# Kernel optimization log

Measured on AMD Instinct MI355X. Metric: run time of the kernel, lower is better.

## Reference

```python
import jax, jax.numpy as jnp
import numpy as np

B = 64; PAST = 128; FUTURE = 64; HID = 64; HEADS = 4
F = 16 + 8 + 24 + 3  # out_preprocess = 51


def _pre(cat, num, emb0, emb1, emb2):
    # pre_processing: embedding lookups per categorical column + last 3 float cols
    return jnp.concatenate([emb0[cat[:, 0]], emb1[cat[:, 1]], emb2[cat[:, 2]], num], axis=-1)


def _gat_conv(x, edge_index, lin_w, att_src, att_dst, bias, heads, out_ch):
    # PyG GATConv: concat=False (head mean), add_self_loops=True, leaky_relu slope 0.2
    N = x.shape[0]
    loops = jnp.arange(N, dtype=edge_index.dtype)
    src = jnp.concatenate([edge_index[0], loops])
    dst = jnp.concatenate([edge_index[1], loops])
    h = (x @ lin_w).reshape(N, heads, out_ch)          # [N, H, C]
    a_src = (h * att_src).sum(-1)                      # [N, H]
    a_dst = (h * att_dst).sum(-1)
    e = jax.nn.leaky_relu(a_src[src] + a_dst[dst], 0.2)  # [E, H]
    m = jax.lax.stop_gradient(jax.ops.segment_max(e, dst, num_segments=N))
    ex = jnp.exp(e - m[dst])
    s = jax.ops.segment_sum(ex, dst, num_segments=N)
    alpha = ex / (s[dst] + 1e-16)                      # softmax over in-edges per node
    out = jax.ops.segment_sum(alpha[:, :, None] * h[src], dst, num_segments=N)
    return out.mean(1) + bias                          # concat=False -> mean over heads


def setup_inputs() -> dict:
    ks = jax.random.split(jax.random.key(0), 17)
    N1, N2 = B * PAST, B * FUTURE
    E1, E2 = N1 * 16, N2 * 16
    return dict(
        cat1=jax.random.randint(ks[0], (N1, 3), 0, 7),
        num1=jax.random.normal(ks[1], (N1, 3), dtype=jnp.float32),
        cat2=jax.random.randint(ks[2], (N2, 3), 0, 7),
        num2=jax.random.normal(ks[3], (N2, 3), dtype=jnp.float32),
        e1=jax.random.randint(ks[4], (2, E1), 0, N1),
        e2=jax.random.randint(ks[5], (2, E2), 0, N2),
        A=jax.random.randint(ks[6], (PAST + FUTURE, PAST + FUTURE), 0, 2),
        emb0=0.1 * jax.random.normal(ks[7], (24, 16), dtype=jnp.float32),
        emb1=0.1 * jax.random.normal(ks[8], (7, 8), dtype=jnp.float32),
        emb2=0.1 * jax.random.normal(ks[9], (500, 24), dtype=jnp.float32),
        g1_lin=0.1 * jax.random.normal(ks[10], (F, HEADS * (F - 1)), dtype=jnp.float32),
        g1_asrc=0.1 * jax.random.normal(ks[11], (HEADS, F - 1), dtype=jnp.float32),
        g1_adst=0.1 * jax.random.normal(ks[12], (HEADS, F - 1), dtype=jnp.float32),
        g1_b=jnp.zeros((F - 1,), dtype=jnp.float32),
        g2_lin=0.1 * jax.random.normal(ks[13], (F, HEADS), dtype=jnp.float32),
        g2_asrc=0.1 * jax.random.normal(ks[14], (HEADS, 1), dtype=jnp.float32),
        g2_adst=0.1 * jax.random.normal(ks[15], (HEADS, 1), dtype=jnp.float32),
        g2_b=jnp.zeros((1,), dtype=jnp.float32),
        W=0.1 * jax.random.normal(ks[16], (F - 1, HID), dtype=jnp.float32),
    )


def reference(cat1, num1, cat2, num2, e1, e2, A, emb0, emb1, emb2,
              g1_lin, g1_asrc, g1_adst, g1_b, g2_lin, g2_asrc, g2_adst, g2_b, W):
    x = _pre(cat1, num1, emb0, emb1, emb2)                       # [B*PAST, F]
    x2 = _pre(cat2, num2, emb0, emb1, emb2).reshape(B, FUTURE, F)
    x1 = _gat_conv(x, e1, g1_lin, g1_asrc, g1_adst, g1_b, HEADS, F - 1).reshape(B, PAST, F - 1)
    # pairwise diff between every (future, past) node pair within a graph
    diff = x1[:, None, :, :] - x2[:, :, None, :F - 1]            # [B, FUTURE, PAST, F-1]
    M = W @ W.T
    M = M + M.T                                                  # WW^T + (WW^T)^T
    # original builds full [PAST, PAST] quadratic form and extracts diagonal;
    # compute only the diagonal: -0.5 * diff_i M diff_i
    alpha = -0.5 * jnp.einsum('bfpd,de,bfpe->bfp', diff, M, diff)
    mask = A[:PAST, PAST:].T                                     # [FUTURE, PAST]
    alpha = jnp.where(mask == 0, -jnp.inf, alpha)
    alpha = jax.nn.softmax(alpha, axis=-1)
    y_past = x.reshape(B, PAST, F)[:, :, -1:]                    # [B, PAST, 1]
    tmp = alpha @ y_past                                         # [B, FUTURE, 1]
    x2b = jnp.concatenate([x2[:, :, :F - 1], tmp], axis=-1)
    out = _gat_conv(x2b.reshape(-1, F), e2, g2_lin, g2_asrc, g2_adst, g2_b, HEADS, 1)
    return out.reshape(B, FUTURE)
```

## Files before the change

### kernel.cpp

```cpp
#include <hip/hip_runtime.h>

static constexpr int B_ = 64, PAST = 128, FUTURE = 64, F_ = 51;
static constexpr int N1 = B_ * PAST;
static constexpr int N2 = B_ * FUTURE;
static constexpr int E1 = N1 * 16;
static constexpr int E2 = N2 * 16;
static constexpr int MAXDEG = 64;
static constexpr int CSR_TOT = E1 + N1 + E2 + N2 + FUTURE * PAST;

__device__ __forceinline__
float node_feat(const int* cat, const float* num, const float* e0, const float* e1,
                const float* e2, int n, int t) {
    if (t < 16) return e0[cat[n * 3 + 0] * 16 + t];
    if (t < 24) return e1[cat[n * 3 + 1] * 8 + (t - 16)];
    if (t < 48) return e2[cat[n * 3 + 2] * 24 + (t - 24)];
    return num[n * 3 + (t - 48)];
}

__global__ __launch_bounds__(256) void k_prep(
        const int* __restrict__ cat1, const float* __restrict__ num1,
        const int* __restrict__ cat2, const float* __restrict__ num2,
        const float* __restrict__ emb0, const float* __restrict__ emb1,
        const float* __restrict__ emb2,
        const float* __restrict__ g1_lin, const float* __restrict__ g1_asrc,
        const float* __restrict__ g1_adst, const float* __restrict__ W,
        float* __restrict__ h1, float* __restrict__ asrc1, float* __restrict__ adst1,
        float* __restrict__ y1, float* __restrict__ x2g, float* __restrict__ P2,
        int* __restrict__ countall) {
    __shared__ float xrow[F_];
    __shared__ float redS[200];
    __shared__ float redD[200];
    int blk = blockIdx.x, t = threadIdx.x;
    if (blk >= N1) {
        int n = blk - N1;
        if (n < 48) countall[n * 256 + t] = 0;
        if (t < F_) {
            float xv = node_feat(cat2, num2, emb0, emb1, emb2, n, t);
            xrow[t] = xv;
            x2g[n * F_ + t] = xv;
        }
        __syncthreads();
        if (t < 64) {
            float acc = 0.f;
            for (int j = 0; j < 50; ++j) acc += xrow[j] * W[j * 64 + t];
            P2[n * 64 + t] = acc;
        }
        return;
    }
    int n = blk;
    if (t < F_) {
        float xv = node_feat(cat1, num1, emb0, emb1, emb2, n, t);
        xrow[t] = xv;
        if (t == 50) y1[n] = xv;
    }
    __syncthreads();
    if (t < 200) {
        float acc = 0.f;
        for (int j = 0; j < F_; ++j) acc += xrow[j] * g1_lin[j * 200 + t];
        h1[n * 200 + t] = acc;
        redS[t] = acc * g1_asrc[t];
        redD[t] = acc * g1_adst[t];
    }
    __syncthreads();
    if (t < 4) {
        float s = 0.f;
        for (int c = 0; c < 50; ++c) s += redS[t * 50 + c];
        asrc1[n * 4 + t] = s;
    } else if (t < 8) {
        int h = t - 4;
        float s = 0.f;
        for (int c = 0; c < 50; ++c) s += redD[h * 50 + c];
        adst1[n * 4 + h] = s;
    }
}

__global__ __launch_bounds__(256) void k_csr(
        const int* __restrict__ e1, const int* __restrict__ e2,
        const int* __restrict__ A,
        int* __restrict__ count1, int* __restrict__ slot1,
        int* __restrict__ count2, int* __restrict__ slot2,
        int* __restrict__ maskT) {
    int i = blockIdx.x * blockDim.x + threadIdx.x;
    if (i < E1) {
        int src = e1[i], dst = e1[E1 + i];
        int pos = atomicAdd(&count1[dst], 1);
        if (pos < MAXDEG) slot1[dst * MAXDEG + pos] = src;
    } else if (i < E1 + N1) {
        int n = i - E1;
        int pos = atomicAdd(&count1[n], 1);
        if (pos < MAXDEG) slot1[n * MAXDEG + pos] = n;
    } else if (i < E1 + N1 + E2) {
        int k = i - E1 - N1;
        int src = e2[k], dst = e2[E2 + k];
        int pos = atomicAdd(&count2[dst], 1);
        if (pos < MAXDEG) slot2[dst * MAXDEG + pos] = src;
    } else if (i < E1 + N1 + E2 + N2) {
        int n = i - E1 - N1 - E2;
        int pos = atomicAdd(&count2[n], 1);
        if (pos < MAXDEG) slot2[n * MAXDEG + pos] = n;
    } else if (i < CSR_TOT) {
        int k = i - (E1 + N1 + E2 + N2);
        int f = k >> 7, pp = k & 127;
        maskT[k] = A[pp * 192 + PAST + f];
    }
}

__global__ __launch_bounds__(256) void k_gat1(
        const int* __restrict__ count1, const int* __restrict__ slot1,
        const float* __restrict__ h1, const float* __restrict__ asrc1,
        const float* __restrict__ adst1, const float* __restrict__ g1_b,
        const float* __restrict__ W, float* __restrict__ P1) {
    __shared__ int   Ssrc[4][64];
    __shared__ float Sw[4][4][64];
    __shared__ float Sx[4][64];
    int t = threadIdx.x, lane = t & 63, wv = t >> 6;
    int n = (blockIdx.x * 256 + t) >> 6;
    int deg = min(count1[n], MAXDEG);
    int my_src = (lane < deg) ? slot1[n * MAXDEG + lane] : 0;
    float ad0 = adst1[n * 4 + 0], ad1 = adst1[n * 4 + 1];
    float ad2 = adst1[n * 4 + 2], ad3 = adst1[n * 4 + 3];
    float ex0 = 0.f, ex1 = 0.f, ex2 = 0.f, ex3 = 0.f;
    if (lane < deg) {
        float e0 = asrc1[my_src * 4 + 0] + ad0;
        float e1 = asrc1[my_src * 4 + 1] + ad1;
        float e2 = asrc1[my_src * 4 + 2] + ad2;
        float e3 = asrc1[my_src * 4 + 3] + ad3;
        e0 = e0 >= 0.f ? e0 : 0.2f * e0;  ex0 = __expf(e0);
        e1 = e1 >= 0.f ? e1 : 0.2f * e1;  ex1 = __expf(e1);
        e2 = e2 >= 0.f ? e2 : 0.2f * e2;  ex2 = __expf(e2);
        e3 = e3 >= 0.f ? e3 : 0.2f * e3;  ex3 = __expf(e3);
    }
    float s0 = ex0, s1 = ex1, s2 = ex2, s3 = ex3;
    #pragma unroll
    for (int m = 32; m >= 1; m >>= 1) {
        s0 += __shfl_xor(s0, m);
        s1 += __shfl_xor(s1, m);
        s2 += __shfl_xor(s2, m);
        s3 += __shfl_xor(s3, m);
    }
    Ssrc[wv][lane] = my_src;
    Sw[wv][0][lane] = ex0 / (s0 + 1e-16f);
    Sw[wv][1][lane] = ex1 / (s1 + 1e-16f);
    Sw[wv][2][lane] = ex2 / (s2 + 1e-16f);
    Sw[wv][3][lane] = ex3 / (s3 + 1e-16f);
    __syncthreads();
    float acc0 = 0.f, acc1 = 0.f, acc2 = 0.f, acc3 = 0.f;
    for (int i = 0; i < deg; ++i) {
        int srci = Ssrc[wv][i];
        float w0 = Sw[wv][0][i], w1 = Sw[wv][1][i];
        float w2 = Sw[wv][2][i], w3 = Sw[wv][3][i];
        if (lane < 50) {
            const float* hr = &h1[srci * 200];
            acc0 += w0 * hr[lane];
            acc1 += w1 * hr[50 + lane];
            acc2 += w2 * hr[100 + lane];
            acc3 += w3 * hr[150 + lane];
        }
    }
    if (lane < 50)
        Sx[wv][lane] = 0.25f * (acc0 + acc1 + acc2 + acc3) + g1_b[lane];
    __syncthreads();
    float a = 0.f;
    for (int j = 0; j < 50; ++j) a += Sx[wv][j] * W[j * 64 + lane];
    P1[n * 64 + lane] = a;
}

__global__ __launch_bounds__(256) void k_attn(
        const float* __restrict__ P1, const float* __restrict__ P2,
        const int* __restrict__ maskT, const float* __restrict__ y1,
        const float* __restrict__ x2g, const float* __restrict__ g2_lin,
        float* __restrict__ h2g) {
    __shared__ float P1s[64 * 129];
    __shared__ float ys[128];
    int b = blockIdx.x >> 2, fg = blockIdx.x & 3;
    int t = threadIdx.x, lane = t & 63, wv = t >> 6;
    const float* P1b = P1 + b * 8192;
    for (int i = t; i < 8192; i += 256) {
        int pp = i >> 6, kk = i & 63;
        P1s[kk * 129 + pp] = P1b[i];
    }
    if (t < 128) ys[t] = y1[b * 128 + t];
    __syncthreads();
    for (int j = 0; j < 4; ++j) {
        int f = fg * 16 + wv * 4 + j;
        int q = b * 64 + f;
        float p2k = P2[q * 64 + lane];
        float d2a = 0.f, d2b = 0.f;
        for (int k = 0; k < 64; ++k) {
            float bk = __shfl(p2k, k);
            float va = P1s[k * 129 + lane] - bk;
            float vb = P1s[k * 129 + 64 + lane] - bk;
            d2a += va * va;
            d2b += vb * vb;
        }
        int ma = maskT[f * 128 + lane];
        int mb = maskT[f * 128 + 64 + lane];
        float va = ma ? -d2a : -1e30f;
        float vb = mb ? -d2b : -1e30f;
        float mx = fmaxf(va, vb);
        #pragma unroll
        for (int m = 32; m >= 1; m >>= 1) mx = fmaxf(mx, __shfl_xor(mx, m));
        float wa = ma ? __expf(va - mx) : 0.f;
        float wb = mb ? __expf(vb - mx) : 0.f;
        float sw = wa + wb;
        float sy = wa * ys[lane] + wb * ys[64 + lane];
        #pragma unroll
        for (int m = 32; m >= 1; m >>= 1) {
            sw += __shfl_xor(sw, m);
            sy += __shfl_xor(sy, m);
        }
        float tsh = sy / sw;
        float xv = (lane < 50) ? x2g[q * F_ + lane] : 0.f;
        #pragma unroll
        for (int h = 0; h < 4; ++h) {
            float c = xv * g2_lin[lane * 4 + h];
            #pragma unroll
            for (int m = 32; m >= 1; m >>= 1) c += __shfl_xor(c, m);
            c += tsh * g2_lin[50 * 4 + h];
            if (lane == h) h2g[q * 4 + h] = c;
        }
    }
}

__global__ __launch_bounds__(256) void k_gat2(
        const int* __restrict__ count2, const int* __restrict__ slot2,
        const float* __restrict__ h2g, const float* __restrict__ g2_asrc,
        const float* __restrict__ g2_adst, const float* __restrict__ g2_b,
        float* __restrict__ out) {
    int wave = (blockIdx.x * blockDim.x + threadIdx.x) >> 6;
    int lane = threadIdx.x & 63;
    if (wave >= N2) return;
    int n = wave;
    int deg = min(count2[n], MAXDEG);
    int my_src = (lane < deg) ? slot2[n * MAXDEG + lane] : 0;
    float ex[4], nm[4], adterm[4], as[4];
    #pragma unroll
    for (int h = 0; h < 4; ++h) {
        as[h] = g2_asrc[h];
        adterm[h] = h2g[n * 4 + h] * g2_adst[h];
        ex[h] = 0.f; nm[h] = 0.f;
    }
    if (lane < deg) {
        #pragma unroll
        for (int h = 0; h < 4; ++h) {
            float hs = h2g[my_src * 4 + h];
            float e = hs * as[h] + adterm[h];
            e = e >= 0.f ? e : 0.2f * e;
            float xv = __expf(e);
            ex[h] = xv;
            nm[h] = xv * hs;
        }
    }
    #pragma unroll
    for (int m = 32; m >= 1; m >>= 1) {
        #pragma unroll
        for (int h = 0; h < 4; ++h) {
            ex[h] += __shfl_xor(ex[h], m);
            nm[h] += __shfl_xor(nm[h], m);
        }
    }
    if (lane == 0) {
        float o = 0.f;
        #pragma unroll
        for (int h = 0; h < 4; ++h) o += nm[h] / (ex[h] + 1e-16f);
        out[n] = 0.25f * o + g2_b[0];
    }
}

extern "C" void kernel_launch(void* const* d_in, const int* in_sizes, int n_in,
                              void* d_out, int out_size, void* d_ws, size_t ws_size,
                              hipStream_t stream) {
    const int*   cat1    = (const int*)  d_in[0];
    const float* num1    = (const float*)d_in[1];
    const int*   cat2    = (const int*)  d_in[2];
    const float* num2    = (const float*)d_in[3];
    const int*   e1      = (const int*)  d_in[4];
    const int*   e2      = (const int*)  d_in[5];
    const int*   A       = (const int*)  d_in[6];
    const float* emb0    = (const float*)d_in[7];
    const float* emb1    = (const float*)d_in[8];
    const float* emb2    = (const float*)d_in[9];
    const float* g1_lin  = (const float*)d_in[10];
    const float* g1_asrc = (const float*)d_in[11];
    const float* g1_adst = (const float*)d_in[12];
    const float* g1_b    = (const float*)d_in[13];
    const float* g2_lin  = (const float*)d_in[14];
    const float* g2_asrc = (const float*)d_in[15];
    const float* g2_adst = (const float*)d_in[16];
    const float* g2_b    = (const float*)d_in[17];
    const float* W       = (const float*)d_in[18];
    float* out = (float*)d_out;

    int*   count1 = (int*)d_ws;
    int*   count2 = count1 + N1;
    int*   slot1  = count2 + N2;
    int*   slot2  = slot1 + N1 * MAXDEG;
    int*   maskT  = slot2 + N2 * MAXDEG;
    float* h1     = (float*)(maskT + FUTURE * PAST);
    float* asrc1  = h1 + N1 * 200;
    float* adst1  = asrc1 + N1 * 4;
    float* y1     = adst1 + N1 * 4;
    float* x2g    = y1 + N1;
    float* P1     = x2g + N2 * F_;
    float* P2     = P1 + N1 * 64;
    float* h2g    = P2 + N2 * 64;

    k_prep<<<N1 + N2, 256, 0, stream>>>(cat1, num1, cat2, num2, emb0, emb1, emb2,
                                        g1_lin, g1_asrc, g1_adst, W,
                                        h1, asrc1, adst1, y1, x2g, P2, count1);
    k_csr<<<CSR_TOT / 256, 256, 0, stream>>>(e1, e2, A, count1, slot1, count2, slot2, maskT);
    k_gat1<<<N1 / 4, 256, 0, stream>>>(count1, slot1, h1, asrc1, adst1, g1_b, W, P1);
    k_attn<<<B_ * 4, 256, 0, stream>>>(P1, P2, maskT, y1, x2g, g2_lin, h2g);
    k_gat2<<<N2 / 4, 256, 0, stream>>>(count2, slot2, h2g, g2_asrc, g2_adst, g2_b, out);
}
```

Measured before the change: 160.3 us.

## Fuse CSR build into prep kernel and expand distance via dot products

Merges the CSR/mask build into the prep kernel as extra blocks, with the degree counters zeroed by a memset beforehand. The future-side linear term for the second GAT is moved into prep. k_gat1 now writes P1 transposed plus per-node squared norms, so k_attn computes 2·dot − |p1|² instead of explicit squared differences (the |p2|² term cancels in the softmax). k_attn loads P1 with float4, uses one future row per wave, and launches 4x more blocks. This saves one launch, removes the transpose in shared memory, and raises parallelism. The cost is strided global writes in gat1 and the numerical differences that come from the norm expansion.

```diff
diff --git a/kernel.cpp b/kernel.cpp
--- a/kernel.cpp
+++ b/kernel.cpp
@@ -7,6 +7,7 @@
 static constexpr int E2 = N2 * 16;
 static constexpr int MAXDEG = 64;
 static constexpr int CSR_TOT = E1 + N1 + E2 + N2 + FUTURE * PAST;
+static constexpr int NB_CSR = CSR_TOT / 256;
 
 __device__ __forceinline__
 float node_feat(const int* cat, const float* num, const float* e0, const float* e1,
@@ -24,16 +25,47 @@
         const float* __restrict__ emb2,
         const float* __restrict__ g1_lin, const float* __restrict__ g1_asrc,
         const float* __restrict__ g1_adst, const float* __restrict__ W,
+        const float* __restrict__ g2_lin,
+        const int* __restrict__ e1, const int* __restrict__ e2,
+        const int* __restrict__ A,
         float* __restrict__ h1, float* __restrict__ asrc1, float* __restrict__ adst1,
         float* __restrict__ y1, float* __restrict__ x2g, float* __restrict__ P2,
-        int* __restrict__ countall) {
+        float* __restrict__ h2b,
+        int* __restrict__ count1, int* __restrict__ slot1,
+        int* __restrict__ count2, int* __restrict__ slot2, int* __restrict__ maskT) {
+    int blk = blockIdx.x, t = threadIdx.x;
+    if (blk < NB_CSR) {
+        int i = blk * 256 + t;
+        if (i < E1) {
+            int src = e1[i], dst = e1[E1 + i];
+            int pos = atomicAdd(&count1[dst], 1);
+            if (pos < MAXDEG) slot1[dst * MAXDEG + pos] = src;
+        } else if (i < E1 + N1) {
+            int n = i - E1;
+            int pos = atomicAdd(&count1[n], 1);
+            if (pos < MAXDEG) slot1[n * MAXDEG + pos] = n;
+        } else if (i < E1 + N1 + E2) {
+            int k = i - E1 - N1;
+            int src = e2[k], dst = e2[E2 + k];
+            int pos = atomicAdd(&count2[dst], 1);
+            if (pos < MAXDEG) slot2[dst * MAXDEG + pos] = src;
+        } else if (i < E1 + N1 + E2 + N2) {
+            int n = i - E1 - N1 - E2;
+            int pos = atomicAdd(&count2[n], 1);
+            if (pos < MAXDEG) slot2[n * MAXDEG + pos] = n;
+        } else if (i < CSR_TOT) {
+            int k = i - (E1 + N1 + E2 + N2);
+            int f = k >> 7, pp = k & 127;
+            maskT[k] = A[pp * 192 + PAST + f];
+        }
+        return;
+    }
     __shared__ float xrow[F_];
     __shared__ float redS[200];
     __shared__ float redD[200];
-    int blk = blockIdx.x, t = threadIdx.x;
-    if (blk >= N1) {
-        int n = blk - N1;
-        if (n < 48) countall[n * 256 + t] = 0;
+    int rb = blk - NB_CSR;
+    if (rb >= N1) {
+        int n = rb - N1;
         if (t < F_) {
             float xv = node_feat(cat2, num2, emb0, emb1, emb2, n, t);
             xrow[t] = xv;
@@ -44,10 +76,15 @@
             float acc = 0.f;
             for (int j = 0; j < 50; ++j) acc += xrow[j] * W[j * 64 + t];
             P2[n * 64 + t] = acc;
+        } else if (t < 68) {
+            int h = t - 64;
+            float acc = 0.f;
+            for (int j = 0; j < 50; ++j) acc += xrow[j] * g2_lin[j * 4 + h];
+            h2b[n * 4 + h] = acc;
         }
         return;
     }
-    int n = blk;
+    int n = rb;
     if (t < F_) {
         float xv = node_feat(cat1, num1, emb0, emb1, emb2, n, t);
         xrow[t] = xv;
@@ -74,45 +111,15 @@
     }
 }
 
-__global__ __launch_bounds__(256) void k_csr(
-        const int* __restrict__ e1, const int* __restrict__ e2,
-        const int* __restrict__ A,
-        int* __restrict__ count1, int* __restrict__ slot1,
-        int* __restrict__ count2, int* __restrict__ slot2,
-        int* __restrict__ maskT) {
-    int i = blockIdx.x * blockDim.x + threadIdx.x;
-    if (i < E1) {
-        int src = e1[i], dst = e1[E1 + i];
-        int pos = atomicAdd(&count1[dst], 1);
-        if (pos < MAXDEG) slot1[dst * MAXDEG + pos] = src;
-    } else if (i < E1 + N1) {
-        int n = i - E1;
-        int pos = atomicAdd(&count1[n], 1);
-        if (pos < MAXDEG) slot1[n * MAXDEG + pos] = n;
-    } else if (i < E1 + N1 + E2) {
-        int k = i - E1 - N1;
-        int src = e2[k], dst = e2[E2 + k];
-        int pos = atomicAdd(&count2[dst], 1);
-        if (pos < MAXDEG) slot2[dst * MAXDEG + pos] = src;
-    } else if (i < E1 + N1 + E2 + N2) {
-        int n = i - E1 - N1 - E2;
-        int pos = atomicAdd(&count2[n], 1);
-        if (pos < MAXDEG) slot2[n * MAXDEG + pos] = n;
-    } else if (i < CSR_TOT) {
-        int k = i - (E1 + N1 + E2 + N2);
-        int f = k >> 7, pp = k & 127;
-        maskT[k] = A[pp * 192 + PAST + f];
-    }
-}
-
 __global__ __launch_bounds__(256) void k_gat1(
         const int* __restrict__ count1, const int* __restrict__ slot1,
         const float* __restrict__ h1, const float* __restrict__ asrc1,
         const float* __restrict__ adst1, const float* __restrict__ g1_b,
-        const float* __restrict__ W, float* __restrict__ P1) {
-    __shared__ int   Ssrc[4][64];
-    __shared__ float Sw[4][4][64];
-    __shared__ float Sx[4][64];
+        const float* __restrict__ W, float* __restrict__ P1T,
+        float* __restrict__ n1w) {
+    __shared__ int    Ssrc[4][64];
+    __shared__ float4 Sw[4][64];
+    __shared__ float  Sx[4][64];
     int t = threadIdx.x, lane = t & 63, wv = t >> 6;
     int n = (blockIdx.x * 256 + t) >> 6;
     int deg = min(count1[n], MAXDEG);
@@ -139,22 +146,19 @@
         s3 += __shfl_xor(s3, m);
     }
     Ssrc[wv][lane] = my_src;
-    Sw[wv][0][lane] = ex0 / (s0 + 1e-16f);
-    Sw[wv][1][lane] = ex1 / (s1 + 1e-16f);
-    Sw[wv][2][lane] = ex2 / (s2 + 1e-16f);
-    Sw[wv][3][lane] = ex3 / (s3 + 1e-16f);
+    Sw[wv][lane] = make_float4(ex0 / (s0 + 1e-16f), ex1 / (s1 + 1e-16f),
+                               ex2 / (s2 + 1e-16f), ex3 / (s3 + 1e-16f));
     __syncthreads();
     float acc0 = 0.f, acc1 = 0.f, acc2 = 0.f, acc3 = 0.f;
     for (int i = 0; i < deg; ++i) {
         int srci = Ssrc[wv][i];
-        float w0 = Sw[wv][0][i], w1 = Sw[wv][1][i];
-        float w2 = Sw[wv][2][i], w3 = Sw[wv][3][i];
+        float4 w = Sw[wv][i];
         if (lane < 50) {
             const float* hr = &h1[srci * 200];
-            acc0 += w0 * hr[lane];
-            acc1 += w1 * hr[50 + lane];
-            acc2 += w2 * hr[100 + lane];
-            acc3 += w3 * hr[150 + lane];
+            acc0 += w.x * hr[lane];
+            acc1 += w.y * hr[50 + lane];
+            acc2 += w.z * hr[100 + lane];
+            acc3 += w.w * hr[150 + lane];
         }
     }
     if (lane < 50)
@@ -162,64 +166,65 @@
     __syncthreads();
     float a = 0.f;
     for (int j = 0; j < 50; ++j) a += Sx[wv][j] * W[j * 64 + lane];
-    P1[n * 64 + lane] = a;
+    int b = n >> 7, p = n & 127;
+    P1T[b * 8192 + lane * 128 + p] = a;
+    float sq = a * a;
+    #pragma unroll
+    for (int m = 32; m >= 1; m >>= 1) sq += __shfl_xor(sq, m);
+    if (lane == 0) n1w[n] = sq;
 }
 
 __global__ __launch_bounds__(256) void k_attn(
-        const float* __restrict__ P1, const float* __restrict__ P2,
+        const float* __restrict__ P1T, const float* __restrict__ P2,
         const int* __restrict__ maskT, const float* __restrict__ y1,
-        const float* __restrict__ x2g, const float* __restrict__ g2_lin,
-        float* __restrict__ h2g) {
-    __shared__ float P1s[64 * 129];
-    __shared__ float ys[128];
-    int b = blockIdx.x >> 2, fg = blockIdx.x & 3;
+        const float* __restrict__ n1w, const float* __restrict__ h2b,
+        const float* __restrict__ g2_lin, float* __restrict__ h2g) {
+    __shared__ __align__(16) float P1s[8192];
+    __shared__ __align__(16) float ys[128];
+    __shared__ __align__(16) float n1s[128];
+    int b = blockIdx.x >> 4, fg = blockIdx.x & 15;
     int t = threadIdx.x, lane = t & 63, wv = t >> 6;
-    const float* P1b = P1 + b * 8192;
-    for (int i = t; i < 8192; i += 256) {
-        int pp = i >> 6, kk = i & 63;
-        P1s[kk * 129 + pp] = P1b[i];
-    }
-    if (t < 128) ys[t] = y1[b * 128 + t];
-    __syncthreads();
-    for (int j = 0; j < 4; ++j) {
-        int f = fg * 16 + wv * 4 + j;
-        int q = b * 64 + f;
-        float p2k = P2[q * 64 + lane];
-        float d2a = 0.f, d2b = 0.f;
-        for (int k = 0; k < 64; ++k) {
-            float bk = __shfl(p2k, k);
-            float va = P1s[k * 129 + lane] - bk;
-            float vb = P1s[k * 129 + 64 + lane] - bk;
-            d2a += va * va;
-            d2b += vb * vb;
-        }
-        int ma = maskT[f * 128 + lane];
-        int mb = maskT[f * 128 + 64 + lane];
-        float va = ma ? -d2a : -1e30f;
-        float vb = mb ? -d2b : -1e30f;
-        float mx = fmaxf(va, vb);
-        #pragma unroll
-        for (int m = 32; m >= 1; m >>= 1) mx = fmaxf(mx, __shfl_xor(mx, m));
-        float wa = ma ? __expf(va - mx) : 0.f;
-        float wb = mb ? __expf(vb - mx) : 0.f;
-        float sw = wa + wb;
-        float sy = wa * ys[lane] + wb * ys[64 + lane];
-        #pragma unroll
-        for (int m = 32; m >= 1; m >>= 1) {
-            sw += __shfl_xor(sw, m);
-            sy += __shfl_xor(sy, m);
-        }
-        float tsh = sy / sw;
-        float xv = (lane < 50) ? x2g[q * F_ + lane] : 0.f;
-        #pragma unroll
-        for (int h = 0; h < 4; ++h) {
-            float c = xv * g2_lin[lane * 4 + h];
-            #pragma unroll
-            for (int m = 32; m >= 1; m >>= 1) c += __shfl_xor(c, m);
-            c += tsh * g2_lin[50 * 4 + h];
-            if (lane == h) h2g[q * 4 + h] = c;
-        }
-    }
+    const float4* src4 = (const float4*)(P1T + b * 8192);
+    float4* dst4 = (float4*)P1s;
+    #pragma unroll
+    for (int i = 0; i < 8; ++i) dst4[t + i * 256] = src4[t + i * 256];
+    if (t < 128) {
+        ys[t]  = y1[b * 128 + t];
+        n1s[t] = n1w[b * 128 + t];
+    }
+    __syncthreads();
+    int f = (fg << 2) + wv;
+    int q = b * 64 + f;
+    float p2k = P2[q * 64 + lane];
+    float dota = 0.f, dotb = 0.f;
+    const float2* P12 = (const float2*)P1s;
+    #pragma unroll
+    for (int k = 0; k < 64; ++k) {
+        float bk = __shfl(p2k, k);
+        float2 v = P12[k * 64 + lane];
+        dota += v.x * bk;
+        dotb += v.y * bk;
+    }
+    int2  mm  = ((const int2*)maskT)[f * 64 + lane];
+    float2 nv = ((const float2*)n1s)[lane];
+    float va = mm.x ? (2.f * dota - nv.x) : -1e30f;
+    float vb = mm.y ? (2.f * dotb - nv.y) : -1e30f;
+    float mx = fmaxf(va, vb);
+    #pragma unroll
+    for (int m = 32; m >= 1; m >>= 1) mx = fmaxf(mx, __shfl_xor(mx, m));
+    float wa = mm.x ? __expf(va - mx) : 0.f;
+    float wb = mm.y ? __expf(vb - mx) : 0.f;
+    float2 yv = ((const float2*)ys)[lane];
+    float sw = wa + wb;
+    float sy = wa * yv.x + wb * yv.y;
+    #pragma unroll
+    for (int m = 32; m >= 1; m >>= 1) {
+        sw += __shfl_xor(sw, m);
+        sy += __shfl_xor(sy, m);
+    }
+    float tsh = sy / sw;
+    if (lane < 4)
+        h2g[q * 4 + lane] = h2b[q * 4 + lane] + tsh * g2_lin[50 * 4 + lane];
 }
 
 __global__ __launch_bounds__(256) void k_gat2(
@@ -301,15 +306,19 @@
     float* adst1  = asrc1 + N1 * 4;
     float* y1     = adst1 + N1 * 4;
     float* x2g    = y1 + N1;
-    float* P1     = x2g + N2 * F_;
-    float* P2     = P1 + N1 * 64;
+    float* P1T    = x2g + N2 * F_;
+    float* P2     = P1T + N1 * 64;
     float* h2g    = P2 + N2 * 64;
-
-    k_prep<<<N1 + N2, 256, 0, stream>>>(cat1, num1, cat2, num2, emb0, emb1, emb2,
-                                        g1_lin, g1_asrc, g1_adst, W,
-                                        h1, asrc1, adst1, y1, x2g, P2, count1);
-    k_csr<<<CSR_TOT / 256, 256, 0, stream>>>(e1, e2, A, count1, slot1, count2, slot2, maskT);
-    k_gat1<<<N1 / 4, 256, 0, stream>>>(count1, slot1, h1, asrc1, adst1, g1_b, W, P1);
-    k_attn<<<B_ * 4, 256, 0, stream>>>(P1, P2, maskT, y1, x2g, g2_lin, h2g);
+    float* n1w    = h2g + N2 * 4;
+    float* h2b    = n1w + N1;
+
+    hipMemsetAsync(count1, 0, (N1 + N2) * sizeof(int), stream);
+    k_prep<<<NB_CSR + N1 + N2, 256, 0, stream>>>(
+        cat1, num1, cat2, num2, emb0, emb1, emb2, g1_lin, g1_asrc, g1_adst, W,
+        g2_lin, e1, e2, A, h1, asrc1, adst1, y1, x2g, P2, h2b,
+        count1, slot1, count2, slot2, maskT);
+    k_gat1<<<N1 / 4, 256, 0, stream>>>(count1, slot1, h1, asrc1, adst1, g1_b, W,
+                                       P1T, n1w);
+    k_attn<<<B_ * 16, 256, 0, stream>>>(P1T, P2, maskT, y1, n1w, h2b, g2_lin, h2g);
     k_gat2<<<N2 / 4, 256, 0, stream>>>(count2, slot2, h2g, g2_asrc, g2_adst, g2_b, out);
 }
```

Measured after the change: 163.6 us. 1.02x slower.
